# Optimization experiments

Hardware: AMD Instinct MI355X
Metric: run time of the kernel (lower is better)

Reference implementation:

```python
import jax, jax.numpy as jnp
import numpy as np

B, L, D = 4, 8192, 1024


def setup_inputs() -> dict:
    key = jax.random.key(0)
    ks = jax.random.split(key, 10)
    s = 1.0 / np.sqrt(D)
    return {
        "x": jax.random.normal(ks[0], (B, L, D), dtype=jnp.float32),
        "w_ln_z": jax.random.uniform(ks[1], (D, D), jnp.float32, -s, s),
        "b_ln_z": jax.random.uniform(ks[2], (D,), jnp.float32, -s, s),
        "w_dt": jax.random.uniform(ks[3], (D, D), jnp.float32, -s, s),
        "b_dt": jax.random.uniform(ks[4], (D,), jnp.float32, -s, s),
        "w_y": jax.random.uniform(ks[5], (D, D), jnp.float32, -s, s),
        "b_y": jax.random.uniform(ks[6], (D,), jnp.float32, -s, s),
        "w_ya": jax.random.uniform(ks[7], (D, D), jnp.float32, -s, s),
        "b_ya": jax.random.uniform(ks[8], (D,), jnp.float32, -s, s),
        "h0": jax.random.normal(ks[9], (D,), dtype=jnp.float32),  # last_hidden_init
    }


def reference(x, w_ln_z, b_ln_z, w_dt, b_dt, w_y, b_y, w_ya, b_ya, h0):
    # torch Linear: y = x @ W.T + b
    dt = jnp.einsum("bld,ed->ble", x, w_dt) + b_dt
    # -softplus(-a) == log_sigmoid(a); -softplus(a) == log_sigmoid(-a)
    ln_z = jax.nn.log_sigmoid(jnp.einsum("bld,ed->ble", x, w_ln_z) + b_ln_z)
    ln_da = jax.nn.log_sigmoid(dt)
    ln_o_da = jax.nn.log_sigmoid(-dt)
    ln_o_da_cumsum = jnp.cumsum(ln_o_da, axis=1)  # [B,L,D]
    # logcumsumexp along sequence dim
    lcse = jax.lax.cumlogsumexp(ln_z + ln_da - ln_o_da_cumsum, axis=1)
    h_inner = jnp.exp(lcse + ln_o_da_cumsum)
    h_cross = jnp.exp(ln_o_da_cumsum) * h0[None, None, :]  # broadcast last_hidden
    h = h_inner + h_cross
    y = (jnp.einsum("bld,ed->ble", h, w_y) + b_y) * jax.nn.silu(
        jnp.einsum("bld,ed->ble", x, w_ya) + b_ya
    )
    return y
```

## Files before the change

### kernel.cpp

```cpp
#include <hip/hip_runtime.h>
#include <stdint.h>

#define DEV __device__ __forceinline__

typedef unsigned short u16;
using f32x4  = __attribute__((ext_vector_type(4))) float;
using bf16x8 = __attribute__((ext_vector_type(8))) short;

constexpr int B_  = 4;
constexpr int L_  = 8192;
constexpr int D_  = 1024;
constexpr int M_  = B_ * L_;
constexpr int K_  = D_;
constexpr int CCH = 128;
constexpr int TCH = L_ / CCH;

DEV u16 f2bf(float f) {
  uint32_t u = __float_as_uint(f);
  u += 0x7fffu + ((u >> 16) & 1u);
  return (u16)(u >> 16);
}
DEV float bf2f(u16 h) { return __uint_as_float(((uint32_t)h) << 16); }

DEV void async16(const void* g, const void* l) {
  __builtin_amdgcn_global_load_lds(
      (const __attribute__((address_space(1))) unsigned int*)g,
      (__attribute__((address_space(3))) unsigned int*)l, 16, 0, 0);
}

__global__ void cvt_kernel(const float* __restrict__ src, u16* __restrict__ dst, int n8) {
  int stride = gridDim.x * blockDim.x;
  for (int i = blockIdx.x * blockDim.x + threadIdx.x; i < n8; i += stride) {
    float4 a = reinterpret_cast<const float4*>(src)[2 * i];
    float4 b = reinterpret_cast<const float4*>(src)[2 * i + 1];
    union { u16 u[8]; uint4 v; } r;
    r.u[0] = f2bf(a.x); r.u[1] = f2bf(a.y); r.u[2] = f2bf(a.z); r.u[3] = f2bf(a.w);
    r.u[4] = f2bf(b.x); r.u[5] = f2bf(b.y); r.u[6] = f2bf(b.z); r.u[7] = f2bf(b.w);
    reinterpret_cast<uint4*>(dst)[i] = r.v;
  }
}

__global__ void cvt_w_kernel(const float* __restrict__ w0, const float* __restrict__ w1,
                             const float* __restrict__ w2, const float* __restrict__ w3,
                             u16* __restrict__ dcat, u16* __restrict__ d3) {
  constexpr int SEG = K_ * D_ / 8;
  int stride = gridDim.x * blockDim.x;
  for (int i = blockIdx.x * blockDim.x + threadIdx.x; i < 4 * SEG; i += stride) {
    int seg = i / SEG, off = i - seg * SEG;
    const float* src = seg == 0 ? w0 : (seg == 1 ? w1 : (seg == 2 ? w2 : w3));
    u16* dst = seg == 3 ? d3 : (dcat + (size_t)seg * K_ * D_);
    float4 a = reinterpret_cast<const float4*>(src)[2 * off];
    float4 b = reinterpret_cast<const float4*>(src)[2 * off + 1];
    union { u16 u[8]; uint4 v; } r;
    r.u[0] = f2bf(a.x); r.u[1] = f2bf(a.y); r.u[2] = f2bf(a.z); r.u[3] = f2bf(a.w);
    r.u[4] = f2bf(b.x); r.u[5] = f2bf(b.y); r.u[6] = f2bf(b.z); r.u[7] = f2bf(b.w);
    reinterpret_cast<uint4*>(dst)[off] = r.v;
  }
}

DEV void gemm_mainloop128(const u16* __restrict__ Ag, const u16* __restrict__ Bg,
                          int m0, int n0, u16* As, u16* Bs, f32x4 acc[4][4]) {
  const int tid  = threadIdx.x;
  const int lane = tid & 63;
  const int wid  = tid >> 6;
  const int wr   = wid >> 1;
  const int wc   = wid & 1;

  int srow[4], scol[4], sdst[4];
#pragma unroll
  for (int t = 0; t < 4; ++t) {
    int l = t * 256 + tid;
    int row = l >> 3, s = l & 7;
    srow[t] = row;
    scol[t] = (s ^ (row & 7)) * 8;
    sdst[t] = l * 8;
  }

  const int g0    = lane >> 4;
  const int arow  = wr * 64 + (lane & 15);
  const int brow  = wc * 64 + (lane & 15);

  for (int kt = 0; kt < K_; kt += 64) {
#pragma unroll
    for (int t = 0; t < 4; ++t) {
      async16(Ag + (size_t)(m0 + srow[t]) * K_ + kt + scol[t], As + sdst[t]);
      async16(Bg + (size_t)(n0 + srow[t]) * K_ + kt + scol[t], Bs + sdst[t]);
    }
    __syncthreads();
#pragma unroll
    for (int kk = 0; kk < 2; ++kk) {
      const int g = kk * 4 + g0;
      bf16x8 af[4], bfr[4];
#pragma unroll
      for (int i = 0; i < 4; ++i) {
        int ra = arow + i * 16;
        int rb = brow + i * 16;
        af[i]  = *reinterpret_cast<const bf16x8*>(As + ra * 64 + ((g ^ (ra & 7)) * 8));
        bfr[i] = *reinterpret_cast<const bf16x8*>(Bs + rb * 64 + ((g ^ (rb & 7)) * 8));
      }
#pragma unroll
      for (int i = 0; i < 4; ++i)
#pragma unroll
        for (int j = 0; j < 4; ++j)
          acc[i][j] = __builtin_amdgcn_mfma_f32_16x16x32_bf16(af[i], bfr[j], acc[i][j], 0, 0, 0);
    }
    __syncthreads();
  }
}

DEV int xcd_swizzle(int bid, int nwg) {
  int cpx = nwg >> 3;
  return (bid & 7) * cpx + (bid >> 3);
}

__global__ __launch_bounds__(256, 4) void gemm_proj_kernel(
    const u16* __restrict__ xb, const u16* __restrict__ Wcat,
    const float* __restrict__ b_dt, const float* __restrict__ b_lnz,
    const float* __restrict__ b_ya,
    u16* __restrict__ dtb, u16* __restrict__ zpb, u16* __restrict__ syab) {
  __shared__ __align__(16) u16 As[128 * 64];
  __shared__ __align__(16) u16 Bs[128 * 64];
  f32x4 acc[4][4] = {};

  constexpr int NT = 3 * D_ / 128;
  int swz = xcd_swizzle(blockIdx.x, gridDim.x);
  const int m0 = (swz / NT) * 128;
  const int n0 = (swz % NT) * 128;
  gemm_mainloop128(xb, Wcat, m0, n0, As, Bs, acc);

  const int tid = threadIdx.x, lane = tid & 63, wid = tid >> 6;
  const int wr = wid >> 1, wc = wid & 1;
  const int proj  = n0 >> 10;
  const int dbase = n0 & 1023;
  const float* bias = proj == 0 ? b_dt : (proj == 1 ? b_lnz : b_ya);
  u16* outp = proj == 0 ? dtb : (proj == 1 ? zpb : syab);
#pragma unroll
  for (int i = 0; i < 4; ++i) {
    int mr = m0 + wr * 64 + i * 16 + (lane >> 4) * 4;
#pragma unroll
    for (int j = 0; j < 4; ++j) {
      int nc = dbase + wc * 64 + j * 16 + (lane & 15);
      float bv = bias[nc];
#pragma unroll
      for (int r = 0; r < 4; ++r) {
        float v = acc[i][j][r] + bv;
        if (proj == 2) v = v / (1.f + __expf(-v));
        outp[(size_t)(mr + r) * D_ + nc] = f2bf(v);
      }
    }
  }
}

__global__ __launch_bounds__(256, 4) void gemm_out_kernel(
    const u16* __restrict__ hb, const u16* __restrict__ Wyb,
    const float* __restrict__ b_y, const u16* __restrict__ syab,
    float* __restrict__ y) {
  __shared__ __align__(16) u16 As[128 * 64];
  __shared__ __align__(16) u16 Bs[128 * 64];
  f32x4 acc[4][4] = {};

  constexpr int NT = D_ / 128;
  int swz = xcd_swizzle(blockIdx.x, gridDim.x);
  const int m0 = (swz / NT) * 128;
  const int n0 = (swz % NT) * 128;
  gemm_mainloop128(hb, Wyb, m0, n0, As, Bs, acc);

  const int tid = threadIdx.x, lane = tid & 63, wid = tid >> 6;
  const int wr = wid >> 1, wc = wid & 1;
#pragma unroll
  for (int i = 0; i < 4; ++i) {
    int mr = m0 + wr * 64 + i * 16 + (lane >> 4) * 4;
#pragma unroll
    for (int j = 0; j < 4; ++j) {
      int nc = n0 + wc * 64 + j * 16 + (lane & 15);
      float bv = b_y[nc];
#pragma unroll
      for (int r = 0; r < 4; ++r) {
        float v = acc[i][j][r] + bv;
        float s = bf2f(syab[(size_t)(mr + r) * D_ + nc]);
        y[(size_t)(mr + r) * D_ + nc] = v * s;
      }
    }
  }
}

__global__ void scan1_kernel(const u16* __restrict__ dtb, const u16* __restrict__ zpb,
                             float* __restrict__ Ach, float* __restrict__ Bch) {
  const int b = blockIdx.x / CCH;
  const int c = blockIdx.x % CCH;
  const int d0 = threadIdx.x * 4;
  const size_t base = ((size_t)(b * L_ + c * TCH)) * D_ + d0;
  float h[4]  = {0.f, 0.f, 0.f, 0.f};
  float Ap[4] = {1.f, 1.f, 1.f, 1.f};
#pragma unroll 4
  for (int t = 0; t < TCH; ++t) {
    ushort4 du = *reinterpret_cast<const ushort4*>(dtb + base + (size_t)t * D_);
    ushort4 zu = *reinterpret_cast<const ushort4*>(zpb + base + (size_t)t * D_);
    const u16* dp = reinterpret_cast<const u16*>(&du);
    const u16* zz = reinterpret_cast<const u16*>(&zu);
#pragma unroll
    for (int q = 0; q < 4; ++q) {
      float dt = bf2f(dp[q]);
      float zv = bf2f(zz[q]);
      float a  = 1.f / (1.f + __expf(dt));
      float da = 1.f - a;
      float z  = 1.f / (1.f + __expf(-zv));
      h[q]  = a * h[q] + z * da;
      Ap[q] *= a;
    }
  }
  const size_t o = ((size_t)(b * CCH + c)) * D_ + d0;
  *reinterpret_cast<float4*>(Ach + o) = make_float4(Ap[0], Ap[1], Ap[2], Ap[3]);
  *reinterpret_cast<float4*>(Bch + o) = make_float4(h[0], h[1], h[2], h[3]);
}

__global__ void scan2_kernel(const float* __restrict__ Ach, const float* __restrict__ Bch,
                             const float* __restrict__ h0, float* __restrict__ Hin) {
  const int b = blockIdx.x >> 2;
  const int d = (blockIdx.x & 3) * 256 + threadIdx.x;
  float carry = h0[d];
  for (int c = 0; c < CCH; ++c) {
    const size_t o = ((size_t)(b * CCH + c)) * D_ + d;
    Hin[o] = carry;
    carry = Ach[o] * carry + Bch[o];
  }
}

__global__ void scan3_kernel(const u16* __restrict__ dtb, const u16* __restrict__ zpb,
                             const float* __restrict__ Hin, u16* __restrict__ hb) {
  const int b = blockIdx.x / CCH;
  const int c = blockIdx.x % CCH;
  const int d0 = threadIdx.x * 4;
  const size_t base = ((size_t)(b * L_ + c * TCH)) * D_ + d0;
  float4 hv = *reinterpret_cast<const float4*>(Hin + ((size_t)(b * CCH + c)) * D_ + d0);
  float h[4] = {hv.x, hv.y, hv.z, hv.w};
#pragma unroll 4
  for (int t = 0; t < TCH; ++t) {
    ushort4 du = *reinterpret_cast<const ushort4*>(dtb + base + (size_t)t * D_);
    ushort4 zu = *reinterpret_cast<const ushort4*>(zpb + base + (size_t)t * D_);
    const u16* dp = reinterpret_cast<const u16*>(&du);
    const u16* zz = reinterpret_cast<const u16*>(&zu);
    ushort4 ov;
    u16* op = reinterpret_cast<u16*>(&ov);
#pragma unroll
    for (int q = 0; q < 4; ++q) {
      float dt = bf2f(dp[q]);
      float zv = bf2f(zz[q]);
      float a  = 1.f / (1.f + __expf(dt));
      float da = 1.f - a;
      float z  = 1.f / (1.f + __expf(-zv));
      h[q] = a * h[q] + z * da;
      op[q] = f2bf(h[q]);
    }
    *reinterpret_cast<ushort4*>(hb + base + (size_t)t * D_) = ov;
  }
}

extern "C" void kernel_launch(void* const* d_in, const int* in_sizes, int n_in,
                              void* d_out, int out_size, void* d_ws, size_t ws_size,
                              hipStream_t stream) {
  const float* x     = (const float*)d_in[0];
  const float* w_lnz = (const float*)d_in[1];
  const float* b_lnz = (const float*)d_in[2];
  const float* w_dt  = (const float*)d_in[3];
  const float* b_dt  = (const float*)d_in[4];
  const float* w_y   = (const float*)d_in[5];
  const float* b_y   = (const float*)d_in[6];
  const float* w_ya  = (const float*)d_in[7];
  const float* b_ya  = (const float*)d_in[8];
  const float* h0    = (const float*)d_in[9];
  float* y = (float*)d_out;

  char* ws = (char*)d_ws;
  const size_t MB = 1024ull * 1024ull;
  u16*   xb   = (u16*)(ws);
  u16*   Wcat = (u16*)(ws + 64 * MB);
  u16*   Wyb  = (u16*)(ws + 70 * MB);
  u16*   dtb  = (u16*)(ws + 72 * MB);
  u16*   zpb  = (u16*)(ws + 136 * MB);
  u16*   syab = (u16*)(ws + 200 * MB);
  u16*   hb   = (u16*)(ws + 264 * MB);
  float* Ach  = (float*)(ws + 328 * MB);
  float* Bch  = (float*)(ws + 330 * MB);
  float* Hin  = (float*)(ws + 332 * MB);

  cvt_kernel<<<2048, 256, 0, stream>>>(x, xb, M_ * K_ / 8);
  cvt_w_kernel<<<1024, 256, 0, stream>>>(w_dt, w_lnz, w_ya, w_y, Wcat, Wyb);

  gemm_proj_kernel<<<(M_ / 128) * (3 * D_ / 128), 256, 0, stream>>>(
      xb, Wcat, b_dt, b_lnz, b_ya, dtb, zpb, syab);

  scan1_kernel<<<B_ * CCH, 256, 0, stream>>>(dtb, zpb, Ach, Bch);
  scan2_kernel<<<16, 256, 0, stream>>>(Ach, Bch, h0, Hin);
  scan3_kernel<<<B_ * CCH, 256, 0, stream>>>(dtb, zpb, Hin, hb);

  gemm_out_kernel<<<(M_ / 128) * (D_ / 128), 256, 0, stream>>>(
      hb, Wyb, b_y, syab, y);
}
```

Baseline: 701.2 us.

## Rewrite GEMM mainloop with 256x256 tiles and double-buffered async LDS pipeline

Replaces the 128x128 single-buffer GEMM mainloop with a 256x256 tile, 512-thread version that splits each K=64 step into two 32-wide halves. Each half is prefetched into a double-buffered LDS ring using explicit vmcnt waits, and the MFMA blocks run at raised priority. The aim is to overlap global-to-LDS loads with matrix math and to raise arithmetic intensity per block in both projection GEMMs. The costs are higher register and LDS use, fewer blocks per CU, the loss of the XOR swizzle on LDS reads (possible bank conflicts), and delicate hand-counted waitcnt logic.

```diff
diff --git a/kernel.cpp b/kernel.cpp
--- a/kernel.cpp
+++ b/kernel.cpp
@@ -14,6 +14,7 @@
 constexpr int K_  = D_;
 constexpr int CCH = 128;
 constexpr int TCH = L_ / CCH;
+constexpr int NKT = K_ / 64;
 
 DEV u16 f2bf(float f) {
   uint32_t u = __float_as_uint(f);
@@ -27,6 +28,12 @@
       (const __attribute__((address_space(1))) unsigned int*)g,
       (__attribute__((address_space(3))) unsigned int*)l, 16, 0, 0);
 }
+
+#define VM8 asm volatile("s_waitcnt vmcnt(8)" ::: "memory")
+#define VM4 asm volatile("s_waitcnt vmcnt(4)" ::: "memory")
+#define VM0 asm volatile("s_waitcnt vmcnt(0)" ::: "memory")
+#define LGKM0 asm volatile("s_waitcnt lgkmcnt(0)" ::: "memory")
+#define BAR() do { __builtin_amdgcn_s_barrier(); asm volatile("" ::: "memory"); } while (0)
 
 __global__ void cvt_kernel(const float* __restrict__ src, u16* __restrict__ dst, int n8) {
   int stride = gridDim.x * blockDim.x;
@@ -58,54 +65,89 @@
   }
 }
 
-DEV void gemm_mainloop128(const u16* __restrict__ Ag, const u16* __restrict__ Bg,
-                          int m0, int n0, u16* As, u16* Bs, f32x4 acc[4][4]) {
-  const int tid  = threadIdx.x;
-  const int lane = tid & 63;
-  const int wid  = tid >> 6;
-  const int wr   = wid >> 1;
-  const int wc   = wid & 1;
-
-  int srow[4], scol[4], sdst[4];
-#pragma unroll
-  for (int t = 0; t < 4; ++t) {
-    int l = t * 256 + tid;
-    int row = l >> 3, s = l & 7;
-    srow[t] = row;
-    scol[t] = (s ^ (row & 7)) * 8;
-    sdst[t] = l * 8;
-  }
-
-  const int g0    = lane >> 4;
-  const int arow  = wr * 64 + (lane & 15);
-  const int brow  = wc * 64 + (lane & 15);
-
-  for (int kt = 0; kt < K_; kt += 64) {
-#pragma unroll
-    for (int t = 0; t < 4; ++t) {
-      async16(Ag + (size_t)(m0 + srow[t]) * K_ + kt + scol[t], As + sdst[t]);
-      async16(Bg + (size_t)(n0 + srow[t]) * K_ + kt + scol[t], Bs + sdst[t]);
-    }
-    __syncthreads();
-#pragma unroll
-    for (int kk = 0; kk < 2; ++kk) {
-      const int g = kk * 4 + g0;
-      bf16x8 af[4], bfr[4];
-#pragma unroll
-      for (int i = 0; i < 4; ++i) {
-        int ra = arow + i * 16;
-        int rb = brow + i * 16;
-        af[i]  = *reinterpret_cast<const bf16x8*>(As + ra * 64 + ((g ^ (ra & 7)) * 8));
-        bfr[i] = *reinterpret_cast<const bf16x8*>(Bs + rb * 64 + ((g ^ (rb & 7)) * 8));
-      }
-#pragma unroll
-      for (int i = 0; i < 4; ++i)
-#pragma unroll
-        for (int j = 0; j < 4; ++j)
-          acc[i][j] = __builtin_amdgcn_mfma_f32_16x16x32_bf16(af[i], bfr[j], acc[i][j], 0, 0, 0);
-    }
-    __syncthreads();
-  }
+
+DEV void stage_half(const u16* __restrict__ G, int row0, int kcol, u16* dst, int tid) {
+#pragma unroll
+  for (int t = 0; t < 2; ++t) {
+    int l = t * 512 + tid;
+    int row = l >> 2, sl = l & 3;
+    async16(G + (size_t)(row0 + row) * K_ + kcol + sl * 8, dst + l * 8);
+  }
+}
+
+DEV void mfma16(f32x4 acc[8][4], const bf16x8 af[4], const bf16x8 bf[4], int h) {
+  __builtin_amdgcn_s_setprio(1);
+#pragma unroll
+  for (int i = 0; i < 4; ++i)
+#pragma unroll
+    for (int j = 0; j < 4; ++j)
+      acc[h * 4 + i][j] =
+          __builtin_amdgcn_mfma_f32_16x16x32_bf16(af[i], bf[j], acc[h * 4 + i][j], 0, 0, 0);
+  __builtin_amdgcn_s_setprio(0);
+}
+
+DEV void gemm_mainloop256(const u16* __restrict__ Ag, const u16* __restrict__ Bg,
+                          int m0, int n0, u16* LdsA, u16* LdsB, f32x4 acc[8][4]) {
+  const int tid = threadIdx.x, lane = tid & 63, wid = tid >> 6;
+  const int wr = wid >> 2, wc = wid & 3;
+  const int g0 = lane >> 4, l15 = lane & 15;
+
+  auto AH = [&](int buf, int kk) { return LdsA + (buf * 2 + kk) * 8192; };
+  auto BH = [&](int buf, int kk) { return LdsB + (buf * 2 + kk) * 8192; };
+
+  stage_half(Ag, m0, 0,  AH(0, 0), tid);
+  stage_half(Bg, n0, 0,  BH(0, 0), tid);
+  stage_half(Ag, m0, 32, AH(0, 1), tid);
+  stage_half(Bg, n0, 32, BH(0, 1), tid);
+  stage_half(Ag, m0, 64, AH(1, 0), tid);
+  stage_half(Bg, n0, 64, BH(1, 0), tid);
+  VM8;
+  BAR();
+
+  const int arow = wr * 128 + l15;
+  const int brow = wc * 64 + l15;
+  bf16x8 af[4], bf[4];
+
+#define LOADA(P, RB)                                                        \
+  _Pragma("unroll") for (int i = 0; i < 4; ++i)                             \
+      af[i] = *reinterpret_cast<const bf16x8*>((P) + (RB + i * 16) * 32 + g0 * 8)
+#define LOADB(P)                                                            \
+  _Pragma("unroll") for (int j = 0; j < 4; ++j)                             \
+      bf[j] = *reinterpret_cast<const bf16x8*>((P) + (brow + j * 16) * 32 + g0 * 8)
+
+  for (int v = 0; v < NKT; ++v) {
+    const int par = v & 1;
+    const u16* Ak0 = AH(par, 0); const u16* Ak1 = AH(par, 1);
+    const u16* Bk0 = BH(par, 0); const u16* Bk1 = BH(par, 1);
+
+    LOADA(Ak0, arow); LOADB(Bk0);
+    if (v + 1 < NKT) stage_half(Ag, m0, (v + 1) * 64 + 32, AH(par ^ 1, 1), tid);
+    LGKM0; __builtin_amdgcn_sched_barrier(0);
+    mfma16(acc, af, bf, 0);
+    BAR();
+
+    LOADA(Ak0, arow + 64);
+    if (v + 1 < NKT) stage_half(Bg, n0, (v + 1) * 64 + 32, BH(par ^ 1, 1), tid);
+    LGKM0; __builtin_amdgcn_sched_barrier(0);
+    mfma16(acc, af, bf, 1);
+    if (v < NKT - 1) { VM8; } else { VM0; }
+    BAR();
+
+    LOADA(Ak1, arow); LOADB(Bk1);
+    if (v + 2 < NKT) stage_half(Ag, m0, (v + 2) * 64, AH(par, 0), tid);
+    LGKM0; __builtin_amdgcn_sched_barrier(0);
+    mfma16(acc, af, bf, 0);
+    BAR();
+
+    LOADA(Ak1, arow + 64);
+    if (v + 2 < NKT) stage_half(Bg, n0, (v + 2) * 64, BH(par, 0), tid);
+    LGKM0; __builtin_amdgcn_sched_barrier(0);
+    mfma16(acc, af, bf, 1);
+    if (v < NKT - 2) { VM8; BAR(); }
+    else if (v == NKT - 2) { VM4; BAR(); }
+  }
+#undef LOADA
+#undef LOADB
 }
 
 DEV int xcd_swizzle(int bid, int nwg) {
@@ -113,30 +155,30 @@
   return (bid & 7) * cpx + (bid >> 3);
 }
 
-__global__ __launch_bounds__(256, 4) void gemm_proj_kernel(
+__global__ __launch_bounds__(512, 2) void gemm_proj_kernel(
     const u16* __restrict__ xb, const u16* __restrict__ Wcat,
     const float* __restrict__ b_dt, const float* __restrict__ b_lnz,
     const float* __restrict__ b_ya,
     u16* __restrict__ dtb, u16* __restrict__ zpb, u16* __restrict__ syab) {
-  __shared__ __align__(16) u16 As[128 * 64];
-  __shared__ __align__(16) u16 Bs[128 * 64];
-  f32x4 acc[4][4] = {};
-
-  constexpr int NT = 3 * D_ / 128;
+  __shared__ __align__(16) u16 LdsA[2 * 2 * 8192];
+  __shared__ __align__(16) u16 LdsB[2 * 2 * 8192];
+  f32x4 acc[8][4] = {};
+
+  constexpr int NT = 3 * D_ / 256;
   int swz = xcd_swizzle(blockIdx.x, gridDim.x);
-  const int m0 = (swz / NT) * 128;
-  const int n0 = (swz % NT) * 128;
-  gemm_mainloop128(xb, Wcat, m0, n0, As, Bs, acc);
+  const int m0 = (swz / NT) * 256;
+  const int n0 = (swz % NT) * 256;
+  gemm_mainloop256(xb, Wcat, m0, n0, LdsA, LdsB, acc);
 
   const int tid = threadIdx.x, lane = tid & 63, wid = tid >> 6;
-  const int wr = wid >> 1, wc = wid & 1;
+  const int wr = wid >> 2, wc = wid & 3;
   const int proj  = n0 >> 10;
   const int dbase = n0 & 1023;
   const float* bias = proj == 0 ? b_dt : (proj == 1 ? b_lnz : b_ya);
   u16* outp = proj == 0 ? dtb : (proj == 1 ? zpb : syab);
 #pragma unroll
-  for (int i = 0; i < 4; ++i) {
-    int mr = m0 + wr * 64 + i * 16 + (lane >> 4) * 4;
+  for (int i = 0; i < 8; ++i) {
+    int mr = m0 + wr * 128 + i * 16 + (lane >> 4) * 4;
 #pragma unroll
     for (int j = 0; j < 4; ++j) {
       int nc = dbase + wc * 64 + j * 16 + (lane & 15);
@@ -151,25 +193,25 @@
   }
 }
 
-__global__ __launch_bounds__(256, 4) void gemm_out_kernel(
+__global__ __launch_bounds__(512, 2) void gemm_out_kernel(
     const u16* __restrict__ hb, const u16* __restrict__ Wyb,
     const float* __restrict__ b_y, const u16* __restrict__ syab,
     float* __restrict__ y) {
-  __shared__ __align__(16) u16 As[128 * 64];
-  __shared__ __align__(16) u16 Bs[128 * 64];
-  f32x4 acc[4][4] = {};
-
-  constexpr int NT = D_ / 128;
+  __shared__ __align__(16) u16 LdsA[2 * 2 * 8192];
+  __shared__ __align__(16) u16 LdsB[2 * 2 * 8192];
+  f32x4 acc[8][4] = {};
+
+  constexpr int NT = D_ / 256;
   int swz = xcd_swizzle(blockIdx.x, gridDim.x);
-  const int m0 = (swz / NT) * 128;
-  const int n0 = (swz % NT) * 128;
-  gemm_mainloop128(hb, Wyb, m0, n0, As, Bs, acc);
+  const int m0 = (swz / NT) * 256;
+  const int n0 = (swz % NT) * 256;
+  gemm_mainloop256(hb, Wyb, m0, n0, LdsA, LdsB, acc);
 
   const int tid = threadIdx.x, lane = tid & 63, wid = tid >> 6;
-  const int wr = wid >> 1, wc = wid & 1;
-#pragma unroll
-  for (int i = 0; i < 4; ++i) {
-    int mr = m0 + wr * 64 + i * 16 + (lane >> 4) * 4;
+  const int wr = wid >> 2, wc = wid & 3;
+#pragma unroll
+  for (int i = 0; i < 8; ++i) {
+    int mr = m0 + wr * 128 + i * 16 + (lane >> 4) * 4;
 #pragma unroll
     for (int j = 0; j < 4; ++j) {
       int nc = n0 + wc * 64 + j * 16 + (lane & 15);
@@ -287,13 +329,13 @@
   cvt_kernel<<<2048, 256, 0, stream>>>(x, xb, M_ * K_ / 8);
   cvt_w_kernel<<<1024, 256, 0, stream>>>(w_dt, w_lnz, w_ya, w_y, Wcat, Wyb);
 
-  gemm_proj_kernel<<<(M_ / 128) * (3 * D_ / 128), 256, 0, stream>>>(
+  gemm_proj_kernel<<<(M_ / 256) * (3 * D_ / 256), 512, 0, stream>>>(
       xb, Wcat, b_dt, b_lnz, b_ya, dtb, zpb, syab);
 
   scan1_kernel<<<B_ * CCH, 256, 0, stream>>>(dtb, zpb, Ach, Bch);
   scan2_kernel<<<16, 256, 0, stream>>>(Ach, Bch, h0, Hin);
   scan3_kernel<<<B_ * CCH, 256, 0, stream>>>(dtb, zpb, Hin, hb);
 
-  gemm_out_kernel<<<(M_ / 128) * (D_ / 128), 256, 0, stream>>>(
+  gemm_out_kernel<<<(M_ / 256) * (D_ / 256), 512, 0, stream>>>(
       hb, Wyb, b_y, syab, y);
 }
```

Result: no change. 711.3 us (+1.4%).
